# Performance work log

Hardware: AMD Instinct MI355X
Metric: run time of the kernel (lower is better)

The kernel has to match this reference:

```python
import jax, jax.numpy as jnp
import numpy as np
from jax.ops import segment_sum

N_NODES = 100000
N_EDGES = 1200000
D = 64


def setup_inputs() -> dict:
    key = jax.random.key(0)
    ks = jax.random.split(key, 6)
    feats = jax.random.normal(ks[0], (N_NODES, D), dtype=jnp.float32)
    src = jax.random.randint(ks[1], (N_EDGES,), 0, N_NODES, dtype=jnp.int32)
    dst = jax.random.randint(ks[2], (N_EDGES,), 0, N_NODES, dtype=jnp.int32)
    # Glorot-style init like DGL GraphConv
    scale = 1.0 / np.sqrt(D)
    W1 = jax.random.normal(ks[3], (D, D), dtype=jnp.float32) * scale
    b1 = jnp.zeros((D,), dtype=jnp.float32)
    W2 = jax.random.normal(ks[4], (D, D), dtype=jnp.float32) * scale
    b2 = jnp.zeros((D,), dtype=jnp.float32)
    return {"feats": feats, "src": src, "dst": dst,
            "W1": W1, "b1": b1, "W2": W2, "b2": b2}


def _graph_conv(x, src, dst, W, b, n_nodes):
    # DGL GraphConv, norm='both': D_out^{-1/2} -> A -> D_in^{-1/2} -> W -> +b
    ones = jnp.ones_like(src, dtype=x.dtype)
    deg_out = segment_sum(ones, src, num_segments=n_nodes)
    deg_in = segment_sum(ones, dst, num_segments=n_nodes)
    norm_out = jax.lax.rsqrt(jnp.maximum(deg_out, 1.0))  # clamp(min=1)
    norm_in = jax.lax.rsqrt(jnp.maximum(deg_in, 1.0))
    h = x * norm_out[:, None]                 # [N, d]
    agg = segment_sum(h[src], dst, num_segments=n_nodes)  # spmm: [N, d]
    agg = agg * norm_in[:, None]
    return agg @ W + b


def reference(feats, src, dst, W1, b1, W2, b2):
    n = feats.shape[0]
    x = jax.nn.relu(_graph_conv(feats, src, dst, W1, b1, n))
    return _graph_conv(x, src, dst, W2, b2, n)
```

## Files before the change

kernel.cpp:

```cpp
#include <hip/hip_runtime.h>
#include <hip/hip_fp16.h>

#define D      64
#define BSHIFT 9
#define BSIZE  512
#define NBMAX  256
#define CAP    8192
#define CHUNK  4096

typedef _Float16 h2 __attribute__((ext_vector_type(2)));
union UH2 { unsigned u; h2 h; };

__device__ __forceinline__ unsigned short f2h(float f) {
    __half h = __float2half_rn(f);
    return *reinterpret_cast<unsigned short*>(&h);
}
__device__ __forceinline__ h2 u2h(unsigned u) { UH2 t; t.u = u; return t.h; }
__device__ __forceinline__ unsigned h2u(h2 h) { UH2 t; t.h = h; return t.u; }

__global__ void __launch_bounds__(256)
binA_kernel(const int* __restrict__ src, const int* __restrict__ dst,
            int* __restrict__ curD, int* __restrict__ curS,
            unsigned int* __restrict__ bufD,
            unsigned short* __restrict__ bufS, int n_edges) {
    __shared__ unsigned int   stD[CHUNK];
    __shared__ unsigned short stS[CHUNK];
    __shared__ unsigned char  stDB[CHUNK], stSB[CHUNK];
    __shared__ int histD[NBMAX], histS[NBMAX];
    __shared__ int offD[NBMAX], offS[NBMAX];
    __shared__ int bgD[NBMAX], bgS[NBMAX];

    int t = threadIdx.x;
    int per = (n_edges + gridDim.x - 1) / gridDim.x;
    int lo = blockIdx.x * per;
    int hi = min(lo + per, n_edges);

    for (int c0 = lo; c0 < hi; c0 += CHUNK) {
        int m = min(CHUNK, hi - c0);
        histD[t] = 0; histS[t] = 0;
        __syncthreads();
        for (int i = t; i < m; i += 256) {
            atomicAdd(&histD[dst[c0 + i] >> BSHIFT], 1);
            atomicAdd(&histS[src[c0 + i] >> BSHIFT], 1);
        }
        __syncthreads();
        int vD = histD[t], vS = histS[t];
        offD[t] = vD; offS[t] = vS;
        __syncthreads();
        for (int o = 1; o < 256; o <<= 1) {
            int xD = (t >= o) ? offD[t - o] : 0;
            int xS = (t >= o) ? offS[t - o] : 0;
            __syncthreads();
            offD[t] += xD; offS[t] += xS;
            __syncthreads();
        }
        offD[t] -= vD; offS[t] -= vS;
        bgD[t] = vD ? atomicAdd(&curD[t], vD) : 0;
        bgS[t] = vS ? atomicAdd(&curS[t], vS) : 0;
        __syncthreads();
        for (int i = t; i < m; i += 256) {
            int s = src[c0 + i], d = dst[c0 + i];
            int bd = d >> BSHIFT;
            int p = atomicAdd(&offD[bd], 1);
            stD[p]  = (unsigned)s | ((unsigned)(d & (BSIZE - 1)) << 17);
            stDB[p] = (unsigned char)bd;
            int bs = s >> BSHIFT;
            int q = atomicAdd(&offS[bs], 1);
            stS[q]  = (unsigned short)(s & (BSIZE - 1));
            stSB[q] = (unsigned char)bs;
        }
        __syncthreads();
        for (int i = t; i < m; i += 256) {
            int bd = stDB[i];
            int lb = offD[bd] - histD[bd];
            int gp = bgD[bd] + (i - lb);
            if (gp < CAP) bufD[(size_t)bd * CAP + gp] = stD[i];
            int bs = stSB[i];
            int lb2 = offS[bs] - histS[bs];
            int gq = bgS[bs] + (i - lb2);
            if (gq < CAP) bufS[(size_t)bs * CAP + gq] = stS[i];
        }
        __syncthreads();
    }
}

__global__ void __launch_bounds__(512)
binBC_kernel(const unsigned int* __restrict__ bufD,
             unsigned int* __restrict__ edgeC,
             const unsigned short* __restrict__ bufS,
             const int* __restrict__ curD, const int* __restrict__ curS,
             int* __restrict__ rp, int* __restrict__ cnt_in,
             float* __restrict__ norm_out, int n_nodes, int nb) {
    __shared__ int hist[BSIZE], off[BSIZE], cnt2[BSIZE];
    __shared__ int stage[CAP];
    int b = blockIdx.x, t = threadIdx.x;

    if (b < nb) {
        hist[t] = 0;
        __syncthreads();
        int m = min(curD[b], CAP);
        for (int e = t; e < m; e += 512)
            atomicAdd(&hist[bufD[(size_t)b * CAP + e] >> 17], 1);
        __syncthreads();
        int v = hist[t];
        off[t] = v;
        __syncthreads();
        for (int o = 1; o < 512; o <<= 1) {
            int x = (t >= o) ? off[t - o] : 0;
            __syncthreads();
            off[t] += x;
            __syncthreads();
        }
        int excl = off[t] - v;
        __syncthreads();
        off[t] = excl;
        cnt2[t] = 0;
        __syncthreads();
        for (int e = t; e < m; e += 512) {
            unsigned w = bufD[(size_t)b * CAP + e];
            int dl = w >> 17;
            int s  = (int)(w & 0x1FFFFu);
            int pos = off[dl] + atomicAdd(&cnt2[dl], 1);
            stage[pos] = s;
        }
        __syncthreads();
        for (int e = t; e < m; e += 512)
            edgeC[(size_t)b * CAP + e] = (unsigned)stage[e];
        int node = (b << BSHIFT) + t;
        if (node < n_nodes) {
            rp[node] = b * CAP + excl;
            cnt_in[node] = v;
        }
    } else {
        int b2 = b - nb;
        hist[t] = 0;
        __syncthreads();
        int m = min(curS[b2], CAP);
        for (int e = t; e < m; e += 512)
            atomicAdd(&hist[bufS[(size_t)b2 * CAP + e]], 1);
        __syncthreads();
        int node = (b2 << BSHIFT) + t;
        if (node < n_nodes)
            norm_out[node] = rsqrtf(fmaxf((float)hist[t], 1.0f));
    }
}

__global__ void scale_kernel(const float* __restrict__ x,
                             const float* __restrict__ norm_out,
                             unsigned int* __restrict__ xp, int n_nodes) {
    int i = blockIdx.x * blockDim.x + threadIdx.x;
    if (i >= n_nodes * 8) return;
    int r = i >> 3;
    float no = norm_out[r];
    const float4* px = (const float4*)x + (size_t)i * 2;
    float4 v0 = px[0], v1 = px[1];
    uint4 o;
    o.x = (unsigned)f2h(v0.x * no) | ((unsigned)f2h(v0.y * no) << 16);
    o.y = (unsigned)f2h(v0.z * no) | ((unsigned)f2h(v0.w * no) << 16);
    o.z = (unsigned)f2h(v1.x * no) | ((unsigned)f2h(v1.y * no) << 16);
    o.w = (unsigned)f2h(v1.z * no) | ((unsigned)f2h(v1.w * no) << 16);
    ((uint4*)xp)[i] = o;
}

template <bool RELU, bool SCALE_OUT, bool OUT_HALF>
__global__ void __launch_bounds__(256)
gatherw_kernel(const unsigned int* __restrict__ xp,
               const int* __restrict__ rp,
               const unsigned int* __restrict__ edgeC,
               const int* __restrict__ cnt_in,
               const float* __restrict__ norm_out,
               const float* __restrict__ W,
               const float* __restrict__ bias,
               void* __restrict__ outv, int n_nodes) {
    int lane = threadIdx.x & 63;
    int g    = lane >> 3, l8 = lane & 7;
    int wid  = (blockIdx.x * blockDim.x + threadIdx.x) >> 6;
    int nw   = (gridDim.x * blockDim.x) >> 6;

    h2 wp[32];
#pragma unroll
    for (int p = 0; p < 32; ++p) {
        h2 h;
        h.x = (_Float16)W[(2 * p) * D + lane];
        h.y = (_Float16)W[(2 * p + 1) * D + lane];
        wp[p] = h;
    }
    float bj = bias[lane];

    for (int r = wid; r < n_nodes; r += nw) {
        int beg = rp[r];
        int deg = cnt_in[r];
        const unsigned int* el = edgeC + beg;

        h2 a0 = (h2)0, a1 = (h2)0, a2 = (h2)0, a3 = (h2)0;
        int e = g;
        for (; e + 8 < deg; e += 16) {
            int s0 = (int)el[e], s1 = (int)el[e + 8];
            uint4 u = *(const uint4*)(xp + (size_t)s0 * 32 + l8 * 4);
            uint4 v = *(const uint4*)(xp + (size_t)s1 * 32 + l8 * 4);
            a0 += u2h(u.x); a1 += u2h(u.y); a2 += u2h(u.z); a3 += u2h(u.w);
            a0 += u2h(v.x); a1 += u2h(v.y); a2 += u2h(v.z); a3 += u2h(v.w);
        }
        for (; e < deg; e += 8) {
            int s0 = (int)el[e];
            uint4 u = *(const uint4*)(xp + (size_t)s0 * 32 + l8 * 4);
            a0 += u2h(u.x); a1 += u2h(u.y); a2 += u2h(u.z); a3 += u2h(u.w);
        }
#pragma unroll
        for (int off = 8; off < 64; off <<= 1) {
            a0 += u2h(__shfl_xor(h2u(a0), off, 64));
            a1 += u2h(__shfl_xor(h2u(a1), off, 64));
            a2 += u2h(__shfl_xor(h2u(a2), off, 64));
            a3 += u2h(__shfl_xor(h2u(a3), off, 64));
        }
        unsigned au[4] = {h2u(a0), h2u(a1), h2u(a2), h2u(a3)};

        float acc = 0.0f;
#pragma unroll
        for (int p = 0; p < 32; ++p) {
            UH2 t;
            t.u = __builtin_amdgcn_readlane(au[p & 3], p >> 2);
            acc = __builtin_amdgcn_fdot2(t.h, wp[p], acc, false);
        }

        float ni = rsqrtf(fmaxf((float)deg, 1.0f));
        float o  = fmaf(acc, ni, bj);
        if (RELU) o = fmaxf(o, 0.0f);
        if (SCALE_OUT) o *= norm_out[r];
        if (OUT_HALF)
            ((unsigned short*)outv)[(size_t)r * D + lane] = f2h(o);
        else
            ((float*)outv)[(size_t)r * D + lane] = o;
    }
}

__global__ void degree_kernel(const int* __restrict__ src,
                              const int* __restrict__ dst,
                              float* __restrict__ deg_out,
                              float* __restrict__ deg_in, int n_edges) {
    int e = blockIdx.x * blockDim.x + threadIdx.x;
    if (e < n_edges) {
        atomicAdd(&deg_out[src[e]], 1.0f);
        atomicAdd(&deg_in[dst[e]], 1.0f);
    }
}
__global__ void norm_kernel(float* __restrict__ deg, int n) {
    int i = blockIdx.x * blockDim.x + threadIdx.x;
    if (i < n) deg[i] = rsqrtf(fmaxf(deg[i], 1.0f));
}
__global__ void spmm_kernel(const float* __restrict__ x,
                            const int* __restrict__ src,
                            const int* __restrict__ dst,
                            const float* __restrict__ norm_out,
                            float* __restrict__ agg, int n_edges) {
    int gid = blockIdx.x * blockDim.x + threadIdx.x;
    int e = gid >> 6, lane = threadIdx.x & 63;
    if (e < n_edges) {
        int s = src[e], d = dst[e];
        atomicAdd(&agg[(size_t)d * D + lane],
                  x[(size_t)s * D + lane] * norm_out[s]);
    }
}
template <bool RELU>
__global__ void gemm_kernel(const float* __restrict__ agg,
                            const float* __restrict__ norm_in,
                            const float* __restrict__ W,
                            const float* __restrict__ b,
                            float* __restrict__ out, int n_nodes) {
    __shared__ float Wl[D * D];
    for (int i = threadIdx.x; i < D * D; i += blockDim.x) Wl[i] = W[i];
    __syncthreads();
    int lane = threadIdx.x & 63, wave = threadIdx.x >> 6;
    int wpb = blockDim.x >> 6;
    float bj = b[lane];
    for (int row = blockIdx.x * wpb + wave; row < n_nodes;
         row += gridDim.x * wpb) {
        float aa = agg[(size_t)row * D + lane] * norm_in[row];
        float acc = bj;
#pragma unroll
        for (int k = 0; k < D; ++k)
            acc = fmaf(__shfl(aa, k, 64), Wl[k * D + lane], acc);
        if (RELU) acc = fmaxf(acc, 0.0f);
        out[(size_t)row * D + lane] = acc;
    }
}

extern "C" void kernel_launch(void* const* d_in, const int* in_sizes, int n_in,
                              void* d_out, int out_size, void* d_ws, size_t ws_size,
                              hipStream_t stream) {
    const float* feats = (const float*)d_in[0];
    const int*   src   = (const int*)  d_in[1];
    const int*   dst   = (const int*)  d_in[2];
    const float* W1    = (const float*)d_in[3];
    const float* b1    = (const float*)d_in[4];
    const float* W2    = (const float*)d_in[5];
    const float* b2    = (const float*)d_in[6];
    float*       out   = (float*)d_out;

    const int n_nodes = in_sizes[0] / D;
    const int n_edges = in_sizes[1];
    const size_t nd = (size_t)n_nodes * D;
    const int nb = (n_nodes + BSIZE - 1) >> BSHIFT;

    size_t bufD_sz = (size_t)nb * CAP * 4;
    size_t bufS_sz = (size_t)nb * CAP * 2;
    size_t need = bufD_sz + bufS_sz + nd * 2 * 2 + (size_t)n_nodes * 12 + 2048;

    if (ws_size >= need && nb <= NBMAX) {
        char* base = (char*)d_ws;
        unsigned int*   bufD = (unsigned int*)base;
        unsigned short* bufS = (unsigned short*)(base + bufD_sz);
        unsigned int*   xp1  = (unsigned int*)(base + bufD_sz + bufS_sz);
        unsigned int*   xa   = (unsigned int*)((char*)xp1 + nd * 2);
        int*   rp       = (int*)((char*)xa + nd * 2);
        int*   cnt_in   = rp + n_nodes;
        float* norm_out = (float*)(cnt_in + n_nodes);
        int*   curD     = (int*)(norm_out + n_nodes);
        int*   curS     = curD + 256;

        hipMemsetAsync(curD, 0, 2048, stream);
        binA_kernel<<<512, 256, 0, stream>>>(src, dst, curD, curS, bufD, bufS,
                                             n_edges);
        binBC_kernel<<<2 * nb, 512, 0, stream>>>(bufD, bufD, bufS, curD, curS,
                                                 rp, cnt_in, norm_out,
                                                 n_nodes, nb);
        scale_kernel<<<(n_nodes * 8 + 255) / 256, 256, 0, stream>>>(
            feats, norm_out, xp1, n_nodes);

        gatherw_kernel<true, true, true><<<3200, 256, 0, stream>>>(
            xp1, rp, bufD, cnt_in, norm_out, W1, b1, xa, n_nodes);
        gatherw_kernel<false, false, false><<<3200, 256, 0, stream>>>(
            xa, rp, bufD, cnt_in, norm_out, W2, b2, out, n_nodes);
        return;
    }

    float* deg_out = (float*)d_ws;
    float* deg_in  = deg_out + n_nodes;
    float* agg     = deg_in + n_nodes;
    float* x       = out;

    hipMemsetAsync(d_ws, 0, (2 * (size_t)n_nodes + nd) * sizeof(float), stream);
    degree_kernel<<<(n_edges + 255) / 256, 256, 0, stream>>>(src, dst, deg_out,
                                                             deg_in, n_edges);
    norm_kernel<<<(2 * n_nodes + 255) / 256, 256, 0, stream>>>(deg_out,
                                                               2 * n_nodes);
    {
        long long threads = (long long)n_edges * 64;
        int blocks = (int)((threads + 255) / 256);
        spmm_kernel<<<blocks, 256, 0, stream>>>(feats, src, dst, deg_out, agg,
                                                n_edges);
    }
    gemm_kernel<true><<<(n_nodes + 3) / 4, 256, 0, stream>>>(agg, deg_in, W1,
                                                             b1, x, n_nodes);
    hipMemsetAsync(agg, 0, nd * sizeof(float), stream);
    {
        long long threads = (long long)n_edges * 64;
        int blocks = (int)((threads + 255) / 256);
        spmm_kernel<<<blocks, 256, 0, stream>>>(x, src, dst, deg_out, agg,
                                                n_edges);
    }
    gemm_kernel<false><<<(n_nodes + 3) / 4, 256, 0, stream>>>(agg, deg_in, W2,
                                                              b2, out, n_nodes);
}
```

Measured before the change: 215.3 us.

## Fuse feature scaling into degree binning and process two nodes per wavefront

The separate scale_kernel is removed, and the source-degree branch of binBC now converts feats to scaled fp16 directly from its shared histogram, which saves a launch and a norm_out round trip. The gather kernel now splits each wavefront into two halves that aggregate two destination nodes at once with 4 edge groups each, then does both 64x64 projections from a single readlane pass. The grid is doubled. This adds per-lane work in the dot-product phase, and the two halves may be unbalanced when their degrees differ.

```diff
diff --git a/kernel.cpp b/kernel.cpp
--- a/kernel.cpp
+++ b/kernel.cpp
@@ -90,7 +90,10 @@
              const unsigned short* __restrict__ bufS,
              const int* __restrict__ curD, const int* __restrict__ curS,
              int* __restrict__ rp, int* __restrict__ cnt_in,
-             float* __restrict__ norm_out, int n_nodes, int nb) {
+             float* __restrict__ norm_out,
+             const float* __restrict__ feats,
+             uint2* __restrict__ xp1,
+             int n_nodes, int nb) {
     __shared__ int hist[BSIZE], off[BSIZE], cnt2[BSIZE];
     __shared__ int stage[CAP];
     int b = blockIdx.x, t = threadIdx.x;
@@ -133,33 +136,27 @@
         }
     } else {
         int b2 = b - nb;
+        int node0 = b2 << BSHIFT;
         hist[t] = 0;
         __syncthreads();
         int m = min(curS[b2], CAP);
         for (int e = t; e < m; e += 512)
             atomicAdd(&hist[bufS[(size_t)b2 * CAP + e]], 1);
         __syncthreads();
-        int node = (b2 << BSHIFT) + t;
+        int node = node0 + t;
         if (node < n_nodes)
             norm_out[node] = rsqrtf(fmaxf((float)hist[t], 1.0f));
-    }
-}
-
-__global__ void scale_kernel(const float* __restrict__ x,
-                             const float* __restrict__ norm_out,
-                             unsigned int* __restrict__ xp, int n_nodes) {
-    int i = blockIdx.x * blockDim.x + threadIdx.x;
-    if (i >= n_nodes * 8) return;
-    int r = i >> 3;
-    float no = norm_out[r];
-    const float4* px = (const float4*)x + (size_t)i * 2;
-    float4 v0 = px[0], v1 = px[1];
-    uint4 o;
-    o.x = (unsigned)f2h(v0.x * no) | ((unsigned)f2h(v0.y * no) << 16);
-    o.y = (unsigned)f2h(v0.z * no) | ((unsigned)f2h(v0.w * no) << 16);
-    o.z = (unsigned)f2h(v1.x * no) | ((unsigned)f2h(v1.y * no) << 16);
-    o.w = (unsigned)f2h(v1.z * no) | ((unsigned)f2h(v1.w * no) << 16);
-    ((uint4*)xp)[i] = o;
+        int m2 = min(BSIZE, n_nodes - node0);
+        for (int i = t; i < m2 * 16; i += 512) {
+            int row = i >> 4, c = i & 15;
+            float no = rsqrtf(fmaxf((float)hist[row], 1.0f));
+            float4 vv = ((const float4*)feats)[(size_t)(node0 + row) * 16 + c];
+            uint2 o;
+            o.x = (unsigned)f2h(vv.x * no) | ((unsigned)f2h(vv.y * no) << 16);
+            o.y = (unsigned)f2h(vv.z * no) | ((unsigned)f2h(vv.w * no) << 16);
+            xp1[(size_t)(node0 + row) * 16 + c] = o;
+        }
+    }
 }
 
 template <bool RELU, bool SCALE_OUT, bool OUT_HALF>
@@ -174,6 +171,8 @@
                void* __restrict__ outv, int n_nodes) {
     int lane = threadIdx.x & 63;
     int g    = lane >> 3, l8 = lane & 7;
+    int half = g >> 2;
+    int g4   = g & 3;
     int wid  = (blockIdx.x * blockDim.x + threadIdx.x) >> 6;
     int nw   = (gridDim.x * blockDim.x) >> 6;
 
@@ -187,27 +186,30 @@
     }
     float bj = bias[lane];
 
-    for (int r = wid; r < n_nodes; r += nw) {
-        int beg = rp[r];
-        int deg = cnt_in[r];
-        const unsigned int* el = edgeC + beg;
+    int npairs = (n_nodes + 1) >> 1;
+    for (int pr = wid; pr < npairs; pr += nw) {
+        int r0 = pr * 2;
+        int rme = r0 + half;
+        int degme = 0, begme = 0;
+        if (rme < n_nodes) { begme = rp[rme]; degme = cnt_in[rme]; }
+        const unsigned int* el = edgeC + begme;
 
         h2 a0 = (h2)0, a1 = (h2)0, a2 = (h2)0, a3 = (h2)0;
-        int e = g;
-        for (; e + 8 < deg; e += 16) {
-            int s0 = (int)el[e], s1 = (int)el[e + 8];
+        int e = g4;
+        for (; e + 4 < degme; e += 8) {
+            int s0 = (int)el[e], s1 = (int)el[e + 4];
             uint4 u = *(const uint4*)(xp + (size_t)s0 * 32 + l8 * 4);
             uint4 v = *(const uint4*)(xp + (size_t)s1 * 32 + l8 * 4);
             a0 += u2h(u.x); a1 += u2h(u.y); a2 += u2h(u.z); a3 += u2h(u.w);
             a0 += u2h(v.x); a1 += u2h(v.y); a2 += u2h(v.z); a3 += u2h(v.w);
         }
-        for (; e < deg; e += 8) {
+        for (; e < degme; e += 4) {
             int s0 = (int)el[e];
             uint4 u = *(const uint4*)(xp + (size_t)s0 * 32 + l8 * 4);
             a0 += u2h(u.x); a1 += u2h(u.y); a2 += u2h(u.z); a3 += u2h(u.w);
         }
 #pragma unroll
-        for (int off = 8; off < 64; off <<= 1) {
+        for (int off = 8; off < 32; off <<= 1) {
             a0 += u2h(__shfl_xor(h2u(a0), off, 64));
             a1 += u2h(__shfl_xor(h2u(a1), off, 64));
             a2 += u2h(__shfl_xor(h2u(a2), off, 64));
@@ -215,22 +217,38 @@
         }
         unsigned au[4] = {h2u(a0), h2u(a1), h2u(a2), h2u(a3)};
 
-        float acc = 0.0f;
+        float accA = 0.0f, accB = 0.0f;
 #pragma unroll
         for (int p = 0; p < 32; ++p) {
-            UH2 t;
-            t.u = __builtin_amdgcn_readlane(au[p & 3], p >> 2);
-            acc = __builtin_amdgcn_fdot2(t.h, wp[p], acc, false);
-        }
-
-        float ni = rsqrtf(fmaxf((float)deg, 1.0f));
-        float o  = fmaf(acc, ni, bj);
-        if (RELU) o = fmaxf(o, 0.0f);
-        if (SCALE_OUT) o *= norm_out[r];
-        if (OUT_HALF)
-            ((unsigned short*)outv)[(size_t)r * D + lane] = f2h(o);
-        else
-            ((float*)outv)[(size_t)r * D + lane] = o;
+            UH2 ta, tb;
+            ta.u = __builtin_amdgcn_readlane(au[p & 3], p >> 2);
+            tb.u = __builtin_amdgcn_readlane(au[p & 3], 32 + (p >> 2));
+            accA = __builtin_amdgcn_fdot2(ta.h, wp[p], accA, false);
+            accB = __builtin_amdgcn_fdot2(tb.h, wp[p], accB, false);
+        }
+
+        int degA = __builtin_amdgcn_readlane(degme, 0);
+        int degB = __builtin_amdgcn_readlane(degme, 32);
+        {
+            float ni = rsqrtf(fmaxf((float)degA, 1.0f));
+            float o  = fmaf(accA, ni, bj);
+            if (RELU) o = fmaxf(o, 0.0f);
+            if (SCALE_OUT) o *= norm_out[r0];
+            if (OUT_HALF)
+                ((unsigned short*)outv)[(size_t)r0 * D + lane] = f2h(o);
+            else
+                ((float*)outv)[(size_t)r0 * D + lane] = o;
+        }
+        if (r0 + 1 < n_nodes) {
+            float ni = rsqrtf(fmaxf((float)degB, 1.0f));
+            float o  = fmaf(accB, ni, bj);
+            if (RELU) o = fmaxf(o, 0.0f);
+            if (SCALE_OUT) o *= norm_out[r0 + 1];
+            if (OUT_HALF)
+                ((unsigned short*)outv)[(size_t)(r0 + 1) * D + lane] = f2h(o);
+            else
+                ((float*)outv)[(size_t)(r0 + 1) * D + lane] = o;
+        }
     }
 }
 
@@ -323,13 +341,12 @@
                                              n_edges);
         binBC_kernel<<<2 * nb, 512, 0, stream>>>(bufD, bufD, bufS, curD, curS,
                                                  rp, cnt_in, norm_out,
+                                                 feats, (uint2*)xp1,
                                                  n_nodes, nb);
-        scale_kernel<<<(n_nodes * 8 + 255) / 256, 256, 0, stream>>>(
-            feats, norm_out, xp1, n_nodes);
-
-        gatherw_kernel<true, true, true><<<3200, 256, 0, stream>>>(
+
+        gatherw_kernel<true, true, true><<<6400, 256, 0, stream>>>(
             xp1, rp, bufD, cnt_in, norm_out, W1, b1, xa, n_nodes);
-        gatherw_kernel<false, false, false><<<3200, 256, 0, stream>>>(
+        gatherw_kernel<false, false, false><<<6400, 256, 0, stream>>>(
             xa, rp, bufD, cnt_in, norm_out, W2, b2, out, n_nodes);
         return;
     }
```

Result: faster. 204.8 us (-4.9%).
